# Kernel optimization log

Measured on AMD Instinct MI355X. Metric: run time of the kernel, lower is better.

## Reference

```python
import jax, jax.numpy as jnp
import numpy as np

D_MODEL = 512
D_K = 64
D_V = 128
H = D_MODEL // D_V  # 4 heads (num_head = d_model // d_v per the source)
B, N = 4, 2048


def setup_inputs() -> dict:
    key = jax.random.key(0)
    k0, k1, k2, k3, k4 = jax.random.split(key, 5)
    s = 0.02
    return {
        "input_x": jax.random.normal(k0, (B, N, D_MODEL), jnp.float32),
        "Wq": jax.random.normal(k1, (D_MODEL, H * D_K), jnp.float32) * s,
        "Wk": jax.random.normal(k2, (D_MODEL, H * D_K), jnp.float32) * s,
        "Wv": jax.random.normal(k3, (D_MODEL, D_MODEL), jnp.float32) * s,
        "Wo": jax.random.normal(k4, (D_MODEL, D_MODEL), jnp.float32) * s,
    }


def reference(input_x, Wq, Wk, Wv, Wo):
    b, n, _ = input_x.shape
    # Contiguous per-head slices in the source == a simple reshape here.
    q = (input_x @ Wq).reshape(b, n, H, D_K)   # [B,N,H,dk]
    k = (input_x @ Wk).reshape(b, n, H, D_K)   # [B,N,H,dk]
    v = (input_x @ Wv).reshape(b, n, H, D_V)   # [B,N,H,dv]
    scale = jnp.sqrt(jnp.float32(D_K))
    scores = jnp.einsum('bqhd,bkhd->bhqk', q, k) / scale  # [B,H,N,N]
    # FAITHFUL quirk: the source uses nn.Softmax() with no dim on a 3D
    # (B,N,N) tensor; PyTorch's legacy dim inference picks dim=0 (batch).
    attn = jax.nn.softmax(scores, axis=0)
    out = jnp.einsum('bhqk,bkhd->bqhd', attn, v).reshape(b, n, H * D_V)
    return out @ Wo
```

## Files before the change

### kernel.cpp

```cpp
#include <hip/hip_runtime.h>
#include <hip/hip_bf16.h>


typedef __attribute__((ext_vector_type(8))) short short8;
typedef __attribute__((ext_vector_type(4))) float floatx4;
typedef unsigned short u16;
typedef unsigned int u32;

#define MFMA16(a, b, c) __builtin_amdgcn_mfma_f32_16x16x32_bf16((a), (b), (c), 0, 0, 0)

__device__ __forceinline__ u16 f2bf(float f) {
    union { float f; unsigned u; } v; v.f = f;
    unsigned r = v.u + 0x7fffu + ((v.u >> 16) & 1u);
    return (u16)(r >> 16);
}

__device__ __forceinline__ float bf2f(u16 b) {
    union { unsigned u; float f; } v; v.u = ((u32)b) << 16;
    return v.f;
}

__device__ __forceinline__ u32 pk2bf(float a, float b) {
#if __has_builtin(__builtin_amdgcn_cvt_pk_bf16_f32)
    typedef __attribute__((ext_vector_type(2))) __bf16 bf16x2;
    union { bf16x2 v; u32 u; } c;
    c.v = __builtin_amdgcn_cvt_pk_bf16_f32(a, b);
    return c.u;
#else
    return (u32)f2bf(a) | ((u32)f2bf(b) << 16);
#endif
}

__device__ __forceinline__ float ex2(float x) {
#if __has_builtin(__builtin_amdgcn_exp2f)
    return __builtin_amdgcn_exp2f(x);
#else
    return exp2f(x);
#endif
}

__device__ __forceinline__ void gload_lds16(const u16* g, u16* l) {
    __builtin_amdgcn_global_load_lds(
        (const __attribute__((address_space(1))) void*)(const void*)g,
        (__attribute__((address_space(3))) void*)(void*)l, 16, 0, 0);
}

__global__ __launch_bounds__(256) void cast_x_kernel(const float* __restrict__ x,
                                                     u16* __restrict__ xb) {
    int i = blockIdx.x * 256 + threadIdx.x;
    float4 v = ((const float4*)x)[i];
    ushort4 o;
    o.x = f2bf(v.x); o.y = f2bf(v.y); o.z = f2bf(v.z); o.w = f2bf(v.w);
    ((ushort4*)xb)[i] = o;
}

__global__ __launch_bounds__(256) void prep_w_kernel(
    const float* __restrict__ Wq, const float* __restrict__ Wk,
    const float* __restrict__ Wv, const float* __restrict__ Wo,
    u16* __restrict__ WallT, u16* __restrict__ WoT) {
    int i = blockIdx.x * 256 + threadIdx.x;
    if (i < 524288) {
        int n = i >> 9, k = i & 511;
        float v;
        if (n < 256)      v = Wq[k * 256 + n] * 0.18033688011f;
        else if (n < 512) v = Wk[k * 256 + (n - 256)];
        else              v = Wv[k * 512 + (n - 512)];
        WallT[i] = f2bf(v);
    } else {
        int j = i - 524288;
        int n = j >> 9, k = j & 511;
        WoT[j] = f2bf(Wo[k * 512 + n]);
    }
}

__global__ __launch_bounds__(256) void gemm_kernel(
    const u16* __restrict__ A, const u16* __restrict__ BT,
    float* __restrict__ Cf, u16* __restrict__ Qp, u16* __restrict__ Kp,
    u16* __restrict__ Vp, int Kdim, int ldc, int mode) {
    __shared__ u16 Asl[128 * 64];
    __shared__ u16 Bsl[128 * 64];
    const int tid = threadIdx.x;
    const int mbase = blockIdx.y * 128;
    const int nbase = blockIdx.x * 128;
    const int wave = tid >> 6, lane = tid & 63;
    const int wm = wave >> 1, wn = wave & 1;
    const int lq = lane & 15, quad = lane >> 4;

    const u16* gA = A + (size_t)(mbase + wave * 32 + (lane >> 3)) * Kdim + (lane & 7) * 8;
    const u16* gB = BT + (size_t)(nbase + wave * 32 + (lane >> 3)) * Kdim + (lane & 7) * 8;
    u16* lA = &Asl[(wave * 32) * 64];
    u16* lB = &Bsl[(wave * 32) * 64];

    const floatx4 z4 = {0.f, 0.f, 0.f, 0.f};
    floatx4 acc[4][4];
#pragma unroll
    for (int i = 0; i < 4; i++)
#pragma unroll
        for (int j = 0; j < 4; j++) acc[i][j] = z4;

    const int nk = Kdim >> 6;
    for (int kk = 0; kk < nk; kk++) {
        const int kb = kk << 6;
        if (kk) __syncthreads();
#pragma unroll
        for (int i = 0; i < 4; i++) {
            gload_lds16(gA + kb + (size_t)(i * 8) * Kdim, lA + (i * 8) * 64);
            gload_lds16(gB + kb + (size_t)(i * 8) * Kdim, lB + (i * 8) * 64);
        }
        __syncthreads();
#pragma unroll
        for (int ki = 0; ki < 2; ki++) {
            short8 af[4], bf[4];
#pragma unroll
            for (int mi = 0; mi < 4; mi++)
                af[mi] = *(const short8*)&Asl[(wm * 64 + mi * 16 + lq) * 64 + ki * 32 + quad * 8];
#pragma unroll
            for (int ni = 0; ni < 4; ni++)
                bf[ni] = *(const short8*)&Bsl[(wn * 64 + ni * 16 + lq) * 64 + ki * 32 + quad * 8];
#pragma unroll
            for (int mi = 0; mi < 4; mi++)
#pragma unroll
                for (int ni = 0; ni < 4; ni++)
                    acc[mi][ni] = MFMA16(af[mi], bf[ni], acc[mi][ni]);
        }
    }
    if (mode == 1) {
#pragma unroll
        for (int mi = 0; mi < 4; mi++)
#pragma unroll
            for (int ni = 0; ni < 4; ni++)
#pragma unroll
                for (int r = 0; r < 4; r++)
                    Cf[(size_t)(mbase + wm * 64 + mi * 16 + quad * 4 + r) * ldc +
                       (nbase + wn * 64 + ni * 16 + lq)] = acc[mi][ni][r];
    } else if (nbase < 256) {
#pragma unroll
        for (int mi = 0; mi < 4; mi++)
#pragma unroll
            for (int ni = 0; ni < 4; ni++) {
                int col = nbase + wn * 64 + ni * 16 + lq;
                int hq = col >> 6, dkc = col & 63;
                int ki = dkc >> 5, qd = (dkc >> 3) & 3, jq = dkc & 7;
#pragma unroll
                for (int r = 0; r < 4; r++) {
                    int row = mbase + wm * 64 + mi * 16 + quad * 4 + r;
                    int b = row >> 11, q = row & 2047;
                    int qs = q >> 4, lqq = q & 15;
                    Qp[((size_t)((((b * 4 + hq) * 128 + qs) * 2 + ki) * 64 +
                                 (qd * 16 + lqq)) << 3) + jq] = f2bf(acc[mi][ni][r]);
                }
            }
    } else if (nbase < 512) {
#pragma unroll
        for (int mi = 0; mi < 4; mi++)
#pragma unroll
            for (int ni = 0; ni < 4; ni++) {
                int colk = nbase + wn * 64 + ni * 16 + lq - 256;
                int h = colk >> 6, dkc = colk & 63;
                int ki = dkc >> 5, quadk = (dkc >> 3) & 3, j = dkc & 7;
#pragma unroll
                for (int r = 0; r < 4; r++) {
                    int row = mbase + wm * 64 + mi * 16 + quad * 4 + r;
                    int b = row >> 11, key = row & 2047;
                    int kt = key >> 6, r6 = key & 63;
                    int half = r6 >> 5, r5 = r6 & 31;
                    int lqk = r5 >> 1, nj = r5 & 1;
                    Kp[((size_t)((((((b * 4 + h) * 32 + kt) * 2 + half) * 2 + nj)
                                  * 2 + ki) * 64 + (quadk * 16 + lqk)) << 3) + j] =
                        f2bf(acc[mi][ni][r]);
                }
            }
    } else {
#pragma unroll
        for (int mi = 0; mi < 4; mi++)
#pragma unroll
            for (int ni = 0; ni < 4; ni++) {
                int dv = nbase + wn * 64 + ni * 16 + lq - 512;
                int h = dv >> 7, r7 = dv & 127;
                int half = r7 >> 6, r6v = r7 & 63;
                int niv = r6v >> 4, lqv = r6v & 15;
#pragma unroll
                for (int r = 0; r < 4; r++) {
                    int row = mbase + wm * 64 + mi * 16 + quad * 4 + r;
                    int b = row >> 11, key = row & 2047;
                    int kt = key >> 6, r6 = key & 63;
                    int w = r6 >> 5, r5 = r6 & 31;
                    int quadv = r5 >> 3, jv = r5 & 7;
                    Vp[((size_t)((((((b * 4 + h) * 32 + kt) * 2 + half) * 4 + niv)
                                  * 2 + w) * 64 + (quadv * 16 + lqv)) << 3) + jv] =
                        f2bf(acc[mi][ni][r]);
                }
            }
    }
}

__global__ __launch_bounds__(512) void attn_kernel(const u16* __restrict__ Qp,
                                                   const u16* __restrict__ Kp,
                                                   const u16* __restrict__ Vp,
                                                   u16* __restrict__ Pp) {
    __shared__ u16 pl[2 * 4 * 4096];
    const int bx = blockIdx.x;
    const int h = bx & 3;
    const int ck = (bx >> 2) & 3;
    const int qt = bx >> 4;
    const int tid = threadIdx.x;
    const int wave = tid >> 6, lane = tid & 63;
    const int mi = wave & 3, half = wave >> 2;
    const int lq = lane & 15, quad = lane >> 4;
    const int q0 = qt * 64 + mi * 16;
    const int qs = qt * 4 + mi;

    short8 aq[4][2];
#pragma unroll
    for (int b = 0; b < 4; b++)
#pragma unroll
        for (int ki = 0; ki < 2; ki++)
            aq[b][ki] = *(const short8*)&Qp[
                ((size_t)((((b * 4 + h) * 128 + qs) * 2 + ki) * 64 + lane) << 3)];

    const floatx4 z4 = {0.f, 0.f, 0.f, 0.f};
    floatx4 oacc[4][4];
#pragma unroll
    for (int b = 0; b < 4; b++)
#pragma unroll
        for (int ni = 0; ni < 4; ni++) oacc[b][ni] = z4;

    for (int kt = ck * 8; kt < ck * 8 + 8; kt++) {
        u16* plb = &pl[((kt & 1) * 4 + mi) * 4096];
        floatx4 s[4][2];
#pragma unroll
        for (int b = 0; b < 4; b++) {
            const u16* kb = Kp +
                ((size_t)((((b * 4 + h) * 32 + kt) * 2 + half) * 2) << 10) +
                lane * 8;
#pragma unroll
            for (int nj = 0; nj < 2; nj++) {
                s[b][nj] = z4;
#pragma unroll
                for (int ki = 0; ki < 2; ki++)
                    s[b][nj] = MFMA16(aq[b][ki],
                                      *(const short8*)(kb + (nj * 2 + ki) * 512),
                                      s[b][nj]);
            }
        }
        short8 vf[4][8];
#pragma unroll
        for (int b = 0; b < 4; b++) {
            const u16* vb = Vp +
                ((size_t)((((b * 4 + h) * 32 + kt) * 2 + half) * 8) << 9) +
                lane * 8;
#pragma unroll
            for (int t = 0; t < 8; t++)
                vf[b][t] = *(const short8*)(vb + t * 512);
        }
#pragma unroll
        for (int r = 0; r < 4; r++) {
            float e0a = ex2(s[0][0][r]), e0b = ex2(s[0][1][r]);
            float e1a = ex2(s[1][0][r]), e1b = ex2(s[1][1][r]);
            float e2a = ex2(s[2][0][r]), e2b = ex2(s[2][1][r]);
            float e3a = ex2(s[3][0][r]), e3b = ex2(s[3][1][r]);
            float ia = __builtin_amdgcn_rcpf(e0a + e1a + e2a + e3a);
            float ib = __builtin_amdgcn_rcpf(e0b + e1b + e2b + e3b);
            int q = quad * 4 + r;
            int col = (half * 32 + 2 * lq) ^ ((q & 7) * 8);
            *(u32*)&plb[(0 * 16 + q) * 64 + col] = pk2bf(e0a * ia, e0b * ib);
            *(u32*)&plb[(1 * 16 + q) * 64 + col] = pk2bf(e1a * ia, e1b * ib);
            *(u32*)&plb[(2 * 16 + q) * 64 + col] = pk2bf(e2a * ia, e2b * ib);
            *(u32*)&plb[(3 * 16 + q) * 64 + col] = pk2bf(e3a * ia, e3b * ib);
        }
        __syncthreads();
        const int sw = (lq & 7) * 8;
#pragma unroll
        for (int b = 0; b < 4; b++) {
            short8 ap0 = *(const short8*)&plb[(b * 16 + lq) * 64 + ((quad * 8) ^ sw)];
            short8 ap1 = *(const short8*)&plb[(b * 16 + lq) * 64 + ((32 + quad * 8) ^ sw)];
#pragma unroll
            for (int ni = 0; ni < 4; ni++) {
                oacc[b][ni] = MFMA16(ap0, vf[b][ni * 2 + 0], oacc[b][ni]);
                oacc[b][ni] = MFMA16(ap1, vf[b][ni * 2 + 1], oacc[b][ni]);
            }
        }
    }
    u16* Pc = Pp + (size_t)ck * (8192 * 512);
#pragma unroll
    for (int b = 0; b < 4; b++)
#pragma unroll
        for (int ni = 0; ni < 4; ni++)
#pragma unroll
            for (int r = 0; r < 4; r++)
                Pc[(size_t)(b * 2048 + q0 + quad * 4 + r) * 512 +
                   h * 128 + half * 64 + ni * 16 + lq] = f2bf(oacc[b][ni][r]);
}

__global__ __launch_bounds__(256) void reduce4_kernel(u16* __restrict__ P) {
    const size_t S = (size_t)8192 * 512;
    size_t i = ((size_t)blockIdx.x * 256 + threadIdx.x) * 8;
    short8 a = *(short8*)&P[i];
    short8 b = *(short8*)&P[i + S];
    short8 c = *(short8*)&P[i + 2 * S];
    short8 d = *(short8*)&P[i + 3 * S];
    short8 o;
#pragma unroll
    for (int j = 0; j < 8; j++) {
        float s = bf2f((u16)a[j]) + bf2f((u16)b[j]) +
                  bf2f((u16)c[j]) + bf2f((u16)d[j]);
        o[j] = (short)f2bf(s);
    }
    *(short8*)&P[i] = o;
}

extern "C" void kernel_launch(void* const* d_in, const int* in_sizes, int n_in,
                              void* d_out, int out_size, void* d_ws, size_t ws_size,
                              hipStream_t stream) {
    const float* x  = (const float*)d_in[0];
    const float* Wq = (const float*)d_in[1];
    const float* Wk = (const float*)d_in[2];
    const float* Wv = (const float*)d_in[3];
    const float* Wo = (const float*)d_in[4];
    float* out = (float*)d_out;

    char* ws = (char*)d_ws;
    u16* Pp    = (u16*)ws;
    u16* Xb    = (u16*)ws;
    u16* WallT = (u16*)(ws + (size_t)8 * 1024 * 1024);
    char* tail = ws + (size_t)32 * 1024 * 1024;
    u16* WoT   = (u16*)tail; tail += (size_t)512 * 512 * 2;
    u16* Qp    = (u16*)tail; tail += (size_t)8192 * 256 * 2;
    u16* Kp    = (u16*)tail; tail += (size_t)8192 * 256 * 2;
    u16* Vp    = (u16*)tail; tail += (size_t)8192 * 512 * 2;

    cast_x_kernel<<<4096, 256, 0, stream>>>(x, Xb);
    prep_w_kernel<<<3072, 256, 0, stream>>>(Wq, Wk, Wv, Wo, WallT, WoT);
    gemm_kernel<<<dim3(8, 64), 256, 0, stream>>>(Xb, WallT, nullptr,
                                                 Qp, Kp, Vp, 512, 0, 2);
    attn_kernel<<<512, 512, 0, stream>>>(Qp, Kp, Vp, Pp);
    reduce4_kernel<<<2048, 256, 0, stream>>>(Pp);
    gemm_kernel<<<dim3(4, 64), 256, 0, stream>>>(Pp, WoT, out,
                                                 nullptr, nullptr, nullptr,
                                                 512, 512, 1);
}
```

Baseline: 189.2 us.

## Stage QKV epilogue through LDS and repartition attention PV work across waves

The QKV projection epilogue now writes the accumulator tile to shared memory, padded to a 132-element stride and transposed for V, then emits each packed Q/K/V fragment with a single 16-byte coalesced store. Before, every bf16 element went to global memory as its own scattered 2-byte write. In the attention kernel, each wave now owns one 16-column slice of the V dimension across all four query sub-tiles instead of 64 columns for one sub-tile. This cuts the per-wave V fragment loads from 32 to 8 per key tile, at the cost of reading P fragments from every wave's LDS region. The extra LDS traffic and the added barriers in the GEMM epilogue are the trade-off.

```diff
diff --git a/kernel.cpp b/kernel.cpp
--- a/kernel.cpp
+++ b/kernel.cpp
@@ -77,8 +77,9 @@
     const u16* __restrict__ A, const u16* __restrict__ BT,
     float* __restrict__ Cf, u16* __restrict__ Qp, u16* __restrict__ Kp,
     u16* __restrict__ Vp, int Kdim, int ldc, int mode) {
-    __shared__ u16 Asl[128 * 64];
-    __shared__ u16 Bsl[128 * 64];
+    __shared__ u16 sm[16896];
+    u16* Asl = sm;
+    u16* Bsl = sm + 8192;
     const int tid = threadIdx.x;
     const int mbase = blockIdx.y * 128;
     const int nbase = blockIdx.x * 128;
@@ -133,64 +134,68 @@
                 for (int r = 0; r < 4; r++)
                     Cf[(size_t)(mbase + wm * 64 + mi * 16 + quad * 4 + r) * ldc +
                        (nbase + wn * 64 + ni * 16 + lq)] = acc[mi][ni][r];
-    } else if (nbase < 256) {
-#pragma unroll
-        for (int mi = 0; mi < 4; mi++)
-#pragma unroll
-            for (int ni = 0; ni < 4; ni++) {
-                int col = nbase + wn * 64 + ni * 16 + lq;
-                int hq = col >> 6, dkc = col & 63;
-                int ki = dkc >> 5, qd = (dkc >> 3) & 3, jq = dkc & 7;
-#pragma unroll
-                for (int r = 0; r < 4; r++) {
-                    int row = mbase + wm * 64 + mi * 16 + quad * 4 + r;
-                    int b = row >> 11, q = row & 2047;
-                    int qs = q >> 4, lqq = q & 15;
-                    Qp[((size_t)((((b * 4 + hq) * 128 + qs) * 2 + ki) * 64 +
-                                 (qd * 16 + lqq)) << 3) + jq] = f2bf(acc[mi][ni][r]);
-                }
+        return;
+    }
+    __syncthreads();
+    const bool vtile = (nbase >= 512);
+#pragma unroll
+    for (int mi = 0; mi < 4; mi++)
+#pragma unroll
+        for (int ni = 0; ni < 4; ni++) {
+            int cl = wn * 64 + ni * 16 + lq;
+#pragma unroll
+            for (int r = 0; r < 4; r++) {
+                int rl = wm * 64 + mi * 16 + quad * 4 + r;
+                if (vtile) sm[cl * 132 + rl] = f2bf(acc[mi][ni][r]);
+                else       sm[rl * 132 + cl] = f2bf(acc[mi][ni][r]);
             }
+        }
+    __syncthreads();
+    const int b = mbase >> 11;
+    const int keyb = mbase & 2047;
+    if (nbase < 256) {
+        const int hq = nbase >> 6;
+        const int qs_base = keyb >> 4;
+#pragma unroll
+        for (int t = 0; t < 8; t++) {
+            int l = wave * 8 + t;
+            int qs2 = l >> 2, h2 = (l >> 1) & 1, ki = l & 1;
+            int qd = lane >> 4, lqq = lane & 15;
+            short8 v = *(const short8*)&sm[(qs2 * 16 + lqq) * 132 + h2 * 64 + ki * 32 + qd * 8];
+            int h = hq + h2;
+            size_t base = ((size_t)(((b * 4 + h) * 128 + (qs_base + qs2)) * 2 + ki) * 64 + lane) << 3;
+            *(short8*)&Qp[base] = v;
+        }
     } else if (nbase < 512) {
-#pragma unroll
-        for (int mi = 0; mi < 4; mi++)
-#pragma unroll
-            for (int ni = 0; ni < 4; ni++) {
-                int colk = nbase + wn * 64 + ni * 16 + lq - 256;
-                int h = colk >> 6, dkc = colk & 63;
-                int ki = dkc >> 5, quadk = (dkc >> 3) & 3, j = dkc & 7;
-#pragma unroll
-                for (int r = 0; r < 4; r++) {
-                    int row = mbase + wm * 64 + mi * 16 + quad * 4 + r;
-                    int b = row >> 11, key = row & 2047;
-                    int kt = key >> 6, r6 = key & 63;
-                    int half = r6 >> 5, r5 = r6 & 31;
-                    int lqk = r5 >> 1, nj = r5 & 1;
-                    Kp[((size_t)((((((b * 4 + h) * 32 + kt) * 2 + half) * 2 + nj)
-                                  * 2 + ki) * 64 + (quadk * 16 + lqk)) << 3) + j] =
-                        f2bf(acc[mi][ni][r]);
-                }
-            }
+        const int hb = (nbase - 256) >> 6;
+        const int ktb = keyb >> 6;
+#pragma unroll
+        for (int t = 0; t < 8; t++) {
+            int l = wave * 8 + t;
+            int kt2 = l >> 4, hf = (l >> 3) & 1, nj = (l >> 2) & 1;
+            int h2 = (l >> 1) & 1, ki = l & 1;
+            int quadk = lane >> 4, lqk = lane & 15;
+            short8 v = *(const short8*)&sm[(kt2 * 64 + hf * 32 + lqk * 2 + nj) * 132 +
+                                           h2 * 64 + ki * 32 + quadk * 8];
+            int h = hb + h2;
+            size_t base = ((size_t)(((((b * 4 + h) * 32 + (ktb + kt2)) * 2 + hf) * 2 + nj)
+                                    * 2 + ki) * 64 + lane) << 3;
+            *(short8*)&Kp[base] = v;
+        }
     } else {
-#pragma unroll
-        for (int mi = 0; mi < 4; mi++)
-#pragma unroll
-            for (int ni = 0; ni < 4; ni++) {
-                int dv = nbase + wn * 64 + ni * 16 + lq - 512;
-                int h = dv >> 7, r7 = dv & 127;
-                int half = r7 >> 6, r6v = r7 & 63;
-                int niv = r6v >> 4, lqv = r6v & 15;
-#pragma unroll
-                for (int r = 0; r < 4; r++) {
-                    int row = mbase + wm * 64 + mi * 16 + quad * 4 + r;
-                    int b = row >> 11, key = row & 2047;
-                    int kt = key >> 6, r6 = key & 63;
-                    int w = r6 >> 5, r5 = r6 & 31;
-                    int quadv = r5 >> 3, jv = r5 & 7;
-                    Vp[((size_t)((((((b * 4 + h) * 32 + kt) * 2 + half) * 4 + niv)
-                                  * 2 + w) * 64 + (quadv * 16 + lqv)) << 3) + jv] =
-                        f2bf(acc[mi][ni][r]);
-                }
-            }
+        const int h = (nbase - 512) >> 7;
+        const int ktb = keyb >> 6;
+#pragma unroll
+        for (int t = 0; t < 8; t++) {
+            int l = wave * 8 + t;
+            int kt2 = l >> 4, hf = (l >> 3) & 1, niv = (l >> 1) & 3, wv = l & 1;
+            int quadv = lane >> 4, lqv = lane & 15;
+            short8 v = *(const short8*)&sm[(hf * 64 + niv * 16 + lqv) * 132 +
+                                           kt2 * 64 + wv * 32 + quadv * 8];
+            size_t base = ((size_t)(((((b * 4 + h) * 32 + (ktb + kt2)) * 2 + hf) * 4 + niv)
+                                    * 2 + wv) * 64 + lane) << 3;
+            *(short8*)&Vp[base] = v;
+        }
     }
 }
 
@@ -206,8 +211,9 @@
     const int tid = threadIdx.x;
     const int wave = tid >> 6, lane = tid & 63;
     const int mi = wave & 3, half = wave >> 2;
+    const int dq = wave;
+    const int half_v = dq >> 2, ni_v = dq & 3;
     const int lq = lane & 15, quad = lane >> 4;
-    const int q0 = qt * 64 + mi * 16;
     const int qs = qt * 4 + mi;
 
     short8 aq[4][2];
@@ -223,10 +229,11 @@
 #pragma unroll
     for (int b = 0; b < 4; b++)
 #pragma unroll
-        for (int ni = 0; ni < 4; ni++) oacc[b][ni] = z4;
+        for (int m2 = 0; m2 < 4; m2++) oacc[b][m2] = z4;
 
     for (int kt = ck * 8; kt < ck * 8 + 8; kt++) {
         u16* plb = &pl[((kt & 1) * 4 + mi) * 4096];
+        u16* plbuf = &pl[(kt & 1) * 4 * 4096];
         floatx4 s[4][2];
 #pragma unroll
         for (int b = 0; b < 4; b++) {
@@ -243,15 +250,14 @@
                                       s[b][nj]);
             }
         }
-        short8 vf[4][8];
+        short8 vf[4][2];
 #pragma unroll
         for (int b = 0; b < 4; b++) {
             const u16* vb = Vp +
-                ((size_t)((((b * 4 + h) * 32 + kt) * 2 + half) * 8) << 9) +
+                ((size_t)(((((b * 4 + h) * 32 + kt) * 2 + half_v) * 4 + ni_v) * 2) << 9) +
                 lane * 8;
-#pragma unroll
-            for (int t = 0; t < 8; t++)
-                vf[b][t] = *(const short8*)(vb + t * 512);
+            vf[b][0] = *(const short8*)vb;
+            vf[b][1] = *(const short8*)(vb + 512);
         }
 #pragma unroll
         for (int r = 0; r < 4; r++) {
@@ -272,12 +278,13 @@
         const int sw = (lq & 7) * 8;
 #pragma unroll
         for (int b = 0; b < 4; b++) {
-            short8 ap0 = *(const short8*)&plb[(b * 16 + lq) * 64 + ((quad * 8) ^ sw)];
-            short8 ap1 = *(const short8*)&plb[(b * 16 + lq) * 64 + ((32 + quad * 8) ^ sw)];
-#pragma unroll
-            for (int ni = 0; ni < 4; ni++) {
-                oacc[b][ni] = MFMA16(ap0, vf[b][ni * 2 + 0], oacc[b][ni]);
-                oacc[b][ni] = MFMA16(ap1, vf[b][ni * 2 + 1], oacc[b][ni]);
+#pragma unroll
+            for (int m2 = 0; m2 < 4; m2++) {
+                const u16* pm = plbuf + m2 * 4096;
+                short8 ap0 = *(const short8*)&pm[(b * 16 + lq) * 64 + ((quad * 8) ^ sw)];
+                short8 ap1 = *(const short8*)&pm[(b * 16 + lq) * 64 + ((32 + quad * 8) ^ sw)];
+                oacc[b][m2] = MFMA16(ap0, vf[b][0], oacc[b][m2]);
+                oacc[b][m2] = MFMA16(ap1, vf[b][1], oacc[b][m2]);
             }
         }
     }
@@ -285,11 +292,11 @@
 #pragma unroll
     for (int b = 0; b < 4; b++)
 #pragma unroll
-        for (int ni = 0; ni < 4; ni++)
+        for (int m2 = 0; m2 < 4; m2++)
 #pragma unroll
             for (int r = 0; r < 4; r++)
-                Pc[(size_t)(b * 2048 + q0 + quad * 4 + r) * 512 +
-                   h * 128 + half * 64 + ni * 16 + lq] = f2bf(oacc[b][ni][r]);
+                Pc[(size_t)(b * 2048 + qt * 64 + m2 * 16 + quad * 4 + r) * 512 +
+                   h * 128 + dq * 16 + lq] = f2bf(oacc[b][m2][r]);
 }
 
 __global__ __launch_bounds__(256) void reduce4_kernel(u16* __restrict__ P) {
```

New measurement: 172.2 us. 1.1x faster.
